# Kernel tuning notes

Measured on AMD Instinct MI355X. Metric: run time of the kernel, lower is better.

Reference implementation:

```python
import jax, jax.numpy as jnp
import numpy as np

# Dimensions (match init_kwargs / input_specs)
N, C_IN, C, H, W = 2, 256, 256, 80, 80
G, KS = 16, 3                 # groups, kernel_size
K = KS * KS                   # sampling points per group
CG = C // G                   # channels per group
PAD, STRIDE, DIL = 1, 1, 1
OFFSET_SCALE = 1.0
EPS = 1e-5                    # BatchNorm2d eps (eval mode)


def setup_inputs() -> dict:
    key = jax.random.key(0)
    ks = jax.random.split(key, 12)
    rn = lambda k, shape, s=0.02: jax.random.normal(k, shape, dtype=jnp.float32) * s
    return {
        "x": jax.random.normal(ks[0], (N, C_IN, H, W), dtype=jnp.float32),
        # Conv(inc, ouc, k=1): 1x1 conv (bias=False) + BN + SiLU
        "w1": rn(ks[1], (C_IN, C)),
        "bn1_g": jnp.ones((C,), jnp.float32), "bn1_b": jnp.zeros((C,), jnp.float32),
        "bn1_m": rn(ks[2], (C,), 0.1),
        "bn1_v": jax.random.uniform(ks[3], (C,), minval=0.5, maxval=1.5, dtype=jnp.float32),
        # DCNv4: value_proj, fused offset_mask, output_proj
        "wv": rn(ks[4], (C, C)), "bv": jnp.zeros((C,), jnp.float32),
        "wom": rn(ks[5], (C, G * K * 3)), "bom": rn(ks[6], (G * K * 3,), 0.1),
        "wo": rn(ks[7], (C, C)), "bo": jnp.zeros((C,), jnp.float32),
        # trailing BatchNorm2d + SiLU
        "bn2_g": jnp.ones((C,), jnp.float32), "bn2_b": jnp.zeros((C,), jnp.float32),
        "bn2_m": rn(ks[8], (C,), 0.1),
        "bn2_v": jax.random.uniform(ks[9], (C,), minval=0.5, maxval=1.5, dtype=jnp.float32),
    }


def _bn(x, g, b, m, v):
    # eval-mode BatchNorm over last (channel) axis
    return (x - m) * jax.lax.rsqrt(v + EPS) * g + b


def _forward(x, w1, bn1_g, bn1_b, bn1_m, bn1_v, wv, bv, wom, bom, wo, bo,
             bn2_g, bn2_b, bn2_m, bn2_v):
    # --- Conv 1x1 + BN + SiLU (channels-last) ---
    h = jnp.einsum('nchw,cd->nhwd', x, w1)                 # (N,H,W,C)
    h = jax.nn.silu(_bn(h, bn1_g, bn1_b, bn1_m, bn1_v))

    # --- DCNv4 ---
    xf = h.reshape(N, H * W, C)
    value = (xf @ wv + bv).reshape(N, H, W, G, CG)         # value projection
    om = (xf @ wom + bom).reshape(N, H, W, G, 3 * K)       # fused offset+mask
    offset = om[..., :2 * K].reshape(N, H, W, G, K, 2) * OFFSET_SCALE  # (x,y) pairs
    mask = om[..., 2 * K:]                                 # (N,H,W,G,K); v4: no softmax

    # sampling pixel coords: p = out_pos*stride - pad + kernel_offset*dil + learned offset
    ky, kx = jnp.meshgrid(jnp.arange(KS), jnp.arange(KS), indexing='ij')
    ky = (ky.reshape(-1) * DIL).astype(jnp.float32)        # (K,)
    kx = (kx.reshape(-1) * DIL).astype(jnp.float32)
    base_y = (jnp.arange(H) * STRIDE - PAD).astype(jnp.float32)
    base_x = (jnp.arange(W) * STRIDE - PAD).astype(jnp.float32)
    py = base_y[None, :, None, None, None] + ky[None, None, None, None, :] + offset[..., 1]
    px = base_x[None, None, :, None, None] + kx[None, None, None, None, :] + offset[..., 0]

    y0 = jnp.floor(py); x0 = jnp.floor(px)
    wy = py - y0;       wx = px - x0
    y0i = y0.astype(jnp.int32); x0i = x0.astype(jnp.int32)
    y1i = y0i + 1;             x1i = x0i + 1

    ni = jnp.arange(N)[:, None, None, None, None]
    gi = jnp.arange(G)[None, None, None, :, None]

    def gather(yi, xi):
        valid = ((yi >= 0) & (yi < H) & (xi >= 0) & (xi < W)).astype(value.dtype)
        v = value[ni, jnp.clip(yi, 0, H - 1), jnp.clip(xi, 0, W - 1), gi]  # (N,H,W,G,K,CG)
        return v, valid

    acc = jnp.zeros((N, H, W, G, CG), dtype=value.dtype)
    for yi, xi, wgt in ((y0i, x0i, (1 - wy) * (1 - wx)),
                        (y0i, x1i, (1 - wy) * wx),
                        (y1i, x0i, wy * (1 - wx)),
                        (y1i, x1i, wy * wx)):
        v, valid = gather(yi, xi)
        acc = acc + jnp.einsum('nhwgk,nhwgkc->nhwgc', mask * wgt * valid, v)

    out = acc.reshape(N, H * W, C) @ wo + bo               # output projection
    out = out.reshape(N, H, W, C)

    # --- BN + SiLU (wrapper tail) ---
    out = jax.nn.silu(_bn(out, bn2_g, bn2_b, bn2_m, bn2_v))
    return jnp.transpose(out, (0, 3, 1, 2))                # (N,C,H,W)


def reference(x, w1, bn1_g, bn1_b, bn1_m, bn1_v, wv, bv, wom, bom, wo, bo,
              bn2_g, bn2_b, bn2_m, bn2_v):
    return _forward(x, w1, bn1_g, bn1_b, bn1_m, bn1_v, wv, bv, wom, bom,
                    wo, bo, bn2_g, bn2_b, bn2_m, bn2_v)
```

## Files before the change

### kernel.cpp

```cpp
#include <hip/hip_runtime.h>
#include <hip/hip_bf16.h>
#include <math.h>

typedef __attribute__((ext_vector_type(8))) short bf16x8;
typedef __attribute__((ext_vector_type(4))) float f32x4;

#define NB   2
#define CC   256
#define HH   80
#define WW   80
#define HWSZ 6400
#define MM   (NB * HWSZ)
#define NCAT 768
#define EPSB 1e-5f

__global__ __launch_bounds__(256) void transpose_x_k(
    const float* __restrict__ in, __hip_bfloat16* __restrict__ outp)
{
    __shared__ float tile[32][33];
    const float* inz = in + (size_t)256 * HWSZ * blockIdx.z;
    __hip_bfloat16* outz = outp + (size_t)HWSZ * 256 * blockIdx.z;
    int bc = blockIdx.x * 32, br = blockIdx.y * 32;
    int tx = threadIdx.x & 31, ty = threadIdx.x >> 5;
#pragma unroll
    for (int i = 0; i < 32; i += 8)
        tile[ty + i][tx] = inz[(size_t)(br + ty + i) * HWSZ + bc + tx];
    __syncthreads();
#pragma unroll
    for (int i = 0; i < 32; i += 8)
        outz[(size_t)(bc + ty + i) * 256 + br + tx] =
            __float2bfloat16(tile[tx][ty + i]);
}

__device__ inline void t32g(const float* __restrict__ in, int inld, int scol0,
                            int ncols, __hip_bfloat16* __restrict__ out,
                            int orow0, int r0, int tid)
{
    __shared__ float tile[32][33];
    int tx = tid & 31, ty = tid >> 5;
#pragma unroll
    for (int i = 0; i < 32; i += 8)
        tile[ty + i][tx] = (tx < ncols)
            ? in[(size_t)(r0 + ty + i) * inld + scol0 + tx] : 0.f;
    __syncthreads();
#pragma unroll
    for (int i = 0; i < 32; i += 8)
        out[(size_t)(orow0 + ty + i) * 256 + r0 + tx] =
            __float2bfloat16(tile[tx][ty + i]);
}

__global__ __launch_bounds__(256) void prep_weights_k(
    const float* __restrict__ w1, const float* __restrict__ wv,
    const float* __restrict__ wom, const float* __restrict__ wo,
    const float* __restrict__ bv, const float* __restrict__ bom,
    __hip_bfloat16* __restrict__ w1T, __hip_bfloat16* __restrict__ BcatT,
    __hip_bfloat16* __restrict__ woT, float* __restrict__ bcat)
{
    int b = blockIdx.x, t = threadIdx.x;
    if (b < 64) {
        t32g(w1, 256, (b >> 3) * 32, 32, w1T, (b >> 3) * 32, (b & 7) * 32, t);
    } else if (b < 128) {
        int b2 = b - 64;
        t32g(wv, 256, (b2 >> 3) * 32, 32, BcatT, (b2 >> 3) * 32, (b2 & 7) * 32, t);
    } else if (b < 192) {
        int b2 = b - 128;
        t32g(wo, 256, (b2 >> 3) * 32, 32, woT, (b2 >> 3) * 32, (b2 & 7) * 32, t);
    } else if (b < 320) {
        int b2 = b - 192;
        int g = b2 >> 3, ct = b2 & 7;
        t32g(wom, 432, g * 27, 27, BcatT + 256 * 256, g * 32, ct * 32, t);
    } else {
        bcat[t] = bv[t];
#pragma unroll
        for (int j = 0; j < 2; ++j) {
            int r = j * 256 + t;
            int g = r >> 5, jj = r & 31;
            bcat[256 + r] = (jj < 27) ? bom[g * 27 + jj] : 0.f;
        }
    }
}

template <int EPI>
__global__ __launch_bounds__(256) void gemm_mfma(
    const short* __restrict__ A, const short* __restrict__ Bt,
    const float* __restrict__ bias,
    const float* __restrict__ bng, const float* __restrict__ bnb,
    const float* __restrict__ bnm, const float* __restrict__ bnv,
    void* __restrict__ Cout, int ldC)
{
    __shared__ __align__(16) char smem[34048];
    short* As = (short*)smem;
    short* Bs = (short*)(smem + 16384);

    const int t = threadIdx.x;
    const int w = t >> 6, l = t & 63;
    const int wr = w >> 1, wc = w & 1;
    const int m0 = blockIdx.x * 128, n0 = blockIdx.y * 128;

    f32x4 acc[4][4] = {};

    for (int k0 = 0; k0 < 256; k0 += 64) {
#pragma unroll
        for (int i = 0; i < 4; ++i) {
            int s = (w << 2) + i;
            int idx = (s << 6) + l;
            int row = idx >> 3, ch = idx & 7;
            const short* ga = A + (size_t)(m0 + row) * 256 + k0 + (ch << 3);
            __builtin_amdgcn_global_load_lds(
                (const __attribute__((address_space(1))) void*)ga,
                (__attribute__((address_space(3))) void*)(As + (s << 9)), 16, 0, 0);
            const short* gb = Bt + (size_t)(n0 + row) * 256 + k0 + (ch << 3);
            __builtin_amdgcn_global_load_lds(
                (const __attribute__((address_space(1))) void*)gb,
                (__attribute__((address_space(3))) void*)(Bs + (s << 9)), 16, 0, 0);
        }
        __syncthreads();
#pragma unroll
        for (int kk = 0; kk < 2; ++kk) {
            bf16x8 af[4], bfr[4];
#pragma unroll
            for (int mi = 0; mi < 4; ++mi)
                af[mi] = *(const bf16x8*)(As + (wr * 64 + mi * 16 + (l & 15)) * 64 +
                                          kk * 32 + ((l >> 4) << 3));
#pragma unroll
            for (int ni = 0; ni < 4; ++ni)
                bfr[ni] = *(const bf16x8*)(Bs + (wc * 64 + ni * 16 + (l & 15)) * 64 +
                                           kk * 32 + ((l >> 4) << 3));
#pragma unroll
            for (int mi = 0; mi < 4; ++mi)
#pragma unroll
                for (int ni = 0; ni < 4; ++ni)
                    acc[mi][ni] = __builtin_amdgcn_mfma_f32_16x16x32_bf16(
                        af[mi], bfr[ni], acc[mi][ni], 0, 0, 0);
        }
        __syncthreads();
    }

    if (EPI == 0) {
#pragma unroll
        for (int ni = 0; ni < 4; ++ni) {
            int chn = n0 + wc * 64 + ni * 16 + (l & 15);
            float bb = bias[chn];
#pragma unroll
            for (int mi = 0; mi < 4; ++mi) {
                int mbase = m0 + wr * 64 + mi * 16 + ((l >> 4) << 2);
#pragma unroll
                for (int j = 0; j < 4; ++j) {
                    float v = acc[mi][ni][j] + bb;
                    ((__hip_bfloat16*)Cout)[(size_t)(mbase + j) * ldC + chn] =
                        __float2bfloat16(v);
                }
            }
        }
    } else if (EPI == 1) {
#pragma unroll
        for (int ni = 0; ni < 4; ++ni) {
            int chn = n0 + wc * 64 + ni * 16 + (l & 15);
            float mu = bnm[chn], iv = rsqrtf(bnv[chn] + EPSB);
            float gm = bng[chn], bt = bnb[chn];
#pragma unroll
            for (int mi = 0; mi < 4; ++mi) {
                int mbase = m0 + wr * 64 + mi * 16 + ((l >> 4) << 2);
#pragma unroll
                for (int j = 0; j < 4; ++j) {
                    float v = acc[mi][ni][j];
                    v = (v - mu) * iv * gm + bt;
                    v = v / (1.f + __expf(-v));
                    ((__hip_bfloat16*)Cout)[(size_t)(mbase + j) * ldC + chn] =
                        __float2bfloat16(v);
                }
            }
        }
    } else {
        float(*CtT)[132] = (float(*)[132])smem;
        const int nimg = m0 / HWSZ;
        const int p0 = m0 % HWSZ;
#pragma unroll
        for (int h2 = 0; h2 < 2; ++h2) {
            if (wc == h2) {
#pragma unroll
                for (int ni = 0; ni < 4; ++ni)
#pragma unroll
                    for (int mi = 0; mi < 4; ++mi)
#pragma unroll
                        for (int j = 0; j < 4; ++j)
                            CtT[ni * 16 + (l & 15)]
                               [wr * 64 + mi * 16 + ((l >> 4) << 2) + j] =
                                   acc[mi][ni][j];
            }
            __syncthreads();
#pragma unroll
            for (int it = 0; it < 8; ++it) {
                int e4 = it * 256 + t;
                int row = e4 >> 5;
                int c4 = e4 & 31;
                int chn = n0 + h2 * 64 + row;
                float bb = bias[chn];
                float mu = bnm[chn], iv = rsqrtf(bnv[chn] + EPSB);
                float gm = bng[chn], bt = bnb[chn];
                f32x4 v = *(f32x4*)&CtT[row][c4 * 4];
#pragma unroll
                for (int j = 0; j < 4; ++j) {
                    float u = v[j] + bb;
                    u = (u - mu) * iv * gm + bt;
                    u = u / (1.f + __expf(-u));
                    v[j] = u;
                }
                *(f32x4*)&((float*)Cout)[(size_t)(nimg * CC + chn) * HWSZ + p0 + c4 * 4] = v;
            }
            __syncthreads();
        }
    }
}

__device__ inline void fma8(float* acc, const __hip_bfloat16* ptr, float wgt)
{
    bf16x8 v = *(const bf16x8*)ptr;
#pragma unroll
    for (int j = 0; j < 8; ++j) {
        union { unsigned u; float f; } cv;
        cv.u = ((unsigned)(unsigned short)v[j]) << 16;
        acc[j] = fmaf(wgt, cv.f, acc[j]);
    }
}

__global__ __launch_bounds__(256) void dcn_sample_k(
    const __hip_bfloat16* __restrict__ C2, __hip_bfloat16* __restrict__ accb)
{
    const int idx = blockIdx.x * 256 + threadIdx.x;
    const int half = idx & 1;
    const int g = (idx >> 1) & 15;
    const int mp = idx >> 5;
    const int p = mp % HWSZ;
    const int n = mp / HWSZ;
    const int y = p / WW, x = p % WW;

    const unsigned* omw =
        (const unsigned*)(C2 + (size_t)mp * NCAT + 256 + g * 32);
    const __hip_bfloat16* vb =
        C2 + (size_t)n * HWSZ * NCAT + g * 16 + half * 8;

    float mk[9];
    {
        unsigned mw[5];
#pragma unroll
        for (int i = 0; i < 5; ++i) mw[i] = omw[9 + i];
#pragma unroll
        for (int i = 0; i < 9; ++i) {
            unsigned w16 = (i & 1) ? (mw[i >> 1] >> 16) : (mw[i >> 1] & 0xffffu);
            union { unsigned u; float f; } cv; cv.u = w16 << 16;
            mk[i] = cv.f;
        }
    }

    float acc[8] = {};
#pragma unroll
    for (int k = 0; k < 9; ++k) {
        unsigned ow = omw[k];
        union { unsigned u; float f; } cx, cy;
        cx.u = (ow & 0xffffu) << 16;
        cy.u = ow & 0xffff0000u;
        float px = (float)(x - 1 + (k % 3)) + cx.f;
        float py = (float)(y - 1 + (k / 3)) + cy.f;
        float fx = floorf(px), fy = floorf(py);
        float wx = px - fx, wy = py - fy;
        int x0 = (int)fx, y0 = (int)fy;
        int x1 = x0 + 1, y1 = y0 + 1;
        float ax0 = ((unsigned)x0 < (unsigned)WW) ? (1.f - wx) : 0.f;
        float ax1 = ((unsigned)x1 < (unsigned)WW) ? wx : 0.f;
        float ay0 = ((unsigned)y0 < (unsigned)HH) ? mk[k] * (1.f - wy) : 0.f;
        float ay1 = ((unsigned)y1 < (unsigned)HH) ? mk[k] * wy : 0.f;
        int xc0 = min(max(x0, 0), WW - 1);
        int xc1 = min(max(x1, 0), WW - 1);
        int yc0 = min(max(y0, 0), HH - 1);
        int yc1 = min(max(y1, 0), HH - 1);
        const __hip_bfloat16* r0 = vb + (size_t)(yc0 * WW) * NCAT;
        const __hip_bfloat16* r1 = vb + (size_t)(yc1 * WW) * NCAT;
        fma8(acc, r0 + (size_t)xc0 * NCAT, ay0 * ax0);
        fma8(acc, r0 + (size_t)xc1 * NCAT, ay0 * ax1);
        fma8(acc, r1 + (size_t)xc0 * NCAT, ay1 * ax0);
        fma8(acc, r1 + (size_t)xc1 * NCAT, ay1 * ax1);
    }

    __hip_bfloat16* op = accb + (size_t)mp * CC + g * 16 + half * 8;
    bf16x8 ov;
#pragma unroll
    for (int j = 0; j < 8; ++j) {
        __hip_bfloat16 b = __float2bfloat16(acc[j]);
        ov[j] = *reinterpret_cast<short*>(&b);
    }
    *(bf16x8*)op = ov;
}

extern "C" void kernel_launch(void* const* d_in, const int* in_sizes, int n_in,
                              void* d_out, int out_size, void* d_ws, size_t ws_size,
                              hipStream_t stream)
{
    const float* x    = (const float*)d_in[0];
    const float* w1   = (const float*)d_in[1];
    const float* bn1g = (const float*)d_in[2];
    const float* bn1b = (const float*)d_in[3];
    const float* bn1m = (const float*)d_in[4];
    const float* bn1v = (const float*)d_in[5];
    const float* wv   = (const float*)d_in[6];
    const float* bv   = (const float*)d_in[7];
    const float* wom  = (const float*)d_in[8];
    const float* bom  = (const float*)d_in[9];
    const float* wo   = (const float*)d_in[10];
    const float* bo   = (const float*)d_in[11];
    const float* bn2g = (const float*)d_in[12];
    const float* bn2b = (const float*)d_in[13];
    const float* bn2m = (const float*)d_in[14];
    const float* bn2v = (const float*)d_in[15];
    float* out = (float*)d_out;

    char* w = (char*)d_ws;
    __hip_bfloat16* xT    = (__hip_bfloat16*)(w);
    __hip_bfloat16* hbuf  = (__hip_bfloat16*)(w + 6553600);
    __hip_bfloat16* C2    = (__hip_bfloat16*)(w + 13107200);
    __hip_bfloat16* accb  = (__hip_bfloat16*)(w + 32768000);
    __hip_bfloat16* w1T   = (__hip_bfloat16*)(w + 39321600);
    __hip_bfloat16* woT   = (__hip_bfloat16*)(w + 39452672);
    __hip_bfloat16* BcatT = (__hip_bfloat16*)(w + 39583744);
    float*          bcat  = (float*)(w + 39976960);

    dim3 blk(256);

    prep_weights_k<<<dim3(321), blk, 0, stream>>>(
        w1, wv, wom, wo, bv, bom, w1T, BcatT, woT, bcat);
    transpose_x_k<<<dim3(200, 8, 2), blk, 0, stream>>>(x, xT);

    gemm_mfma<1><<<dim3(100, 2), blk, 0, stream>>>(
        (const short*)xT, (const short*)w1T, nullptr,
        bn1g, bn1b, bn1m, bn1v, hbuf, CC);
    gemm_mfma<0><<<dim3(100, 6), blk, 0, stream>>>(
        (const short*)hbuf, (const short*)BcatT, bcat,
        nullptr, nullptr, nullptr, nullptr, C2, NCAT);
    dcn_sample_k<<<dim3(MM * 32 / 256), blk, 0, stream>>>(C2, accb);
    gemm_mfma<2><<<dim3(100, 2), blk, 0, stream>>>(
        (const short*)accb, (const short*)woT, bo,
        bn2g, bn2b, bn2m, bn2v, out, 0);
}
```

Before: 151.4 us.

## Double-buffer GEMM K-loop, halve M tile, and give each DCN thread a full group

The MFMA GEMM now uses a 64x128 tile with double-buffered LDS staging, issuing the next K-slice's async global-to-LDS loads before computing the current one, and it launches twice as many blocks. This aims to hide load latency and raise occupancy on a GPU with many compute units, at the cost of more LDS per block and lower per-block reuse. The deformable sampling kernel now has one thread handle all 16 channels of a group instead of two threads handling 8 each. This halves the redundant offset and mask decoding and bilinear index math, but leaves fewer threads in flight.

Result: no change. 150.6 us (-0.5%).

```diff
diff --git a/kernel.cpp b/kernel.cpp
--- a/kernel.cpp
+++ b/kernel.cpp
@@ -88,51 +88,71 @@
     const float* __restrict__ bnm, const float* __restrict__ bnv,
     void* __restrict__ Cout, int ldC)
 {
-    __shared__ __align__(16) char smem[34048];
+    __shared__ __align__(16) char smem[49152];
     short* As = (short*)smem;
     short* Bs = (short*)(smem + 16384);
 
     const int t = threadIdx.x;
     const int w = t >> 6, l = t & 63;
     const int wr = w >> 1, wc = w & 1;
-    const int m0 = blockIdx.x * 128, n0 = blockIdx.y * 128;
-
-    f32x4 acc[4][4] = {};
-
-    for (int k0 = 0; k0 < 256; k0 += 64) {
-#pragma unroll
-        for (int i = 0; i < 4; ++i) {
-            int s = (w << 2) + i;
-            int idx = (s << 6) + l;
-            int row = idx >> 3, ch = idx & 7;
+    const int m0 = blockIdx.x * 64, n0 = blockIdx.y * 128;
+
+    f32x4 acc[2][4] = {};
+
+    auto STAGE = [&](int b, int k0) {
+        short* AsB = As + b * 4096;
+        short* BsB = Bs + b * 8192;
+#pragma unroll
+        for (int i = 0; i < 2; ++i) {
+            int s = (w << 1) + i;
+            int c = (s << 6) + l;
+            int row = c >> 3, ch = c & 7;
             const short* ga = A + (size_t)(m0 + row) * 256 + k0 + (ch << 3);
             __builtin_amdgcn_global_load_lds(
                 (const __attribute__((address_space(1))) void*)ga,
-                (__attribute__((address_space(3))) void*)(As + (s << 9)), 16, 0, 0);
+                (__attribute__((address_space(3))) void*)(AsB + (s << 9)), 16, 0, 0);
+        }
+#pragma unroll
+        for (int i = 0; i < 4; ++i) {
+            int s = (w << 2) + i;
+            int c = (s << 6) + l;
+            int row = c >> 3, ch = c & 7;
             const short* gb = Bt + (size_t)(n0 + row) * 256 + k0 + (ch << 3);
             __builtin_amdgcn_global_load_lds(
                 (const __attribute__((address_space(1))) void*)gb,
-                (__attribute__((address_space(3))) void*)(Bs + (s << 9)), 16, 0, 0);
-        }
-        __syncthreads();
+                (__attribute__((address_space(3))) void*)(BsB + (s << 9)), 16, 0, 0);
+        }
+    };
+
+    auto COMPUTE = [&](int b) {
+        const short* AsB = As + b * 4096;
+        const short* BsB = Bs + b * 8192;
 #pragma unroll
         for (int kk = 0; kk < 2; ++kk) {
-            bf16x8 af[4], bfr[4];
-#pragma unroll
-            for (int mi = 0; mi < 4; ++mi)
-                af[mi] = *(const bf16x8*)(As + (wr * 64 + mi * 16 + (l & 15)) * 64 +
+            bf16x8 af[2], bfr[4];
+#pragma unroll
+            for (int mi = 0; mi < 2; ++mi)
+                af[mi] = *(const bf16x8*)(AsB + (wr * 32 + mi * 16 + (l & 15)) * 64 +
                                           kk * 32 + ((l >> 4) << 3));
 #pragma unroll
             for (int ni = 0; ni < 4; ++ni)
-                bfr[ni] = *(const bf16x8*)(Bs + (wc * 64 + ni * 16 + (l & 15)) * 64 +
+                bfr[ni] = *(const bf16x8*)(BsB + (wc * 64 + ni * 16 + (l & 15)) * 64 +
                                            kk * 32 + ((l >> 4) << 3));
 #pragma unroll
-            for (int mi = 0; mi < 4; ++mi)
+            for (int mi = 0; mi < 2; ++mi)
 #pragma unroll
                 for (int ni = 0; ni < 4; ++ni)
                     acc[mi][ni] = __builtin_amdgcn_mfma_f32_16x16x32_bf16(
                         af[mi], bfr[ni], acc[mi][ni], 0, 0, 0);
         }
+    };
+
+    STAGE(0, 0);
+    __syncthreads();
+#pragma unroll
+    for (int tt = 0; tt < 4; ++tt) {
+        if (tt < 3) STAGE((tt + 1) & 1, (tt + 1) * 64);
+        COMPUTE(tt & 1);
         __syncthreads();
     }
 
@@ -142,8 +162,8 @@
             int chn = n0 + wc * 64 + ni * 16 + (l & 15);
             float bb = bias[chn];
 #pragma unroll
-            for (int mi = 0; mi < 4; ++mi) {
-                int mbase = m0 + wr * 64 + mi * 16 + ((l >> 4) << 2);
+            for (int mi = 0; mi < 2; ++mi) {
+                int mbase = m0 + wr * 32 + mi * 16 + ((l >> 4) << 2);
 #pragma unroll
                 for (int j = 0; j < 4; ++j) {
                     float v = acc[mi][ni][j] + bb;
@@ -159,8 +179,8 @@
             float mu = bnm[chn], iv = rsqrtf(bnv[chn] + EPSB);
             float gm = bng[chn], bt = bnb[chn];
 #pragma unroll
-            for (int mi = 0; mi < 4; ++mi) {
-                int mbase = m0 + wr * 64 + mi * 16 + ((l >> 4) << 2);
+            for (int mi = 0; mi < 2; ++mi) {
+                int mbase = m0 + wr * 32 + mi * 16 + ((l >> 4) << 2);
 #pragma unroll
                 for (int j = 0; j < 4; ++j) {
                     float v = acc[mi][ni][j];
@@ -172,7 +192,7 @@
             }
         }
     } else {
-        float(*CtT)[132] = (float(*)[132])smem;
+        float(*CtT)[68] = (float(*)[68])smem;
         const int nimg = m0 / HWSZ;
         const int p0 = m0 % HWSZ;
 #pragma unroll
@@ -181,19 +201,19 @@
 #pragma unroll
                 for (int ni = 0; ni < 4; ++ni)
 #pragma unroll
-                    for (int mi = 0; mi < 4; ++mi)
+                    for (int mi = 0; mi < 2; ++mi)
 #pragma unroll
                         for (int j = 0; j < 4; ++j)
                             CtT[ni * 16 + (l & 15)]
-                               [wr * 64 + mi * 16 + ((l >> 4) << 2) + j] =
+                               [wr * 32 + mi * 16 + ((l >> 4) << 2) + j] =
                                    acc[mi][ni][j];
             }
             __syncthreads();
 #pragma unroll
-            for (int it = 0; it < 8; ++it) {
+            for (int it = 0; it < 4; ++it) {
                 int e4 = it * 256 + t;
-                int row = e4 >> 5;
-                int c4 = e4 & 31;
+                int row = e4 >> 4;
+                int c4 = e4 & 15;
                 int chn = n0 + h2 * 64 + row;
                 float bb = bias[chn];
                 float mu = bnm[chn], iv = rsqrtf(bnv[chn] + EPSB);
@@ -213,14 +233,21 @@
     }
 }
 
-__device__ inline void fma8(float* acc, const __hip_bfloat16* ptr, float wgt)
-{
-    bf16x8 v = *(const bf16x8*)ptr;
+__device__ inline void fma16(float* acc, const __hip_bfloat16* ptr, float wgt)
+{
+    bf16x8 v0 = *(const bf16x8*)ptr;
+    bf16x8 v1 = *(const bf16x8*)(ptr + 8);
 #pragma unroll
     for (int j = 0; j < 8; ++j) {
         union { unsigned u; float f; } cv;
-        cv.u = ((unsigned)(unsigned short)v[j]) << 16;
+        cv.u = ((unsigned)(unsigned short)v0[j]) << 16;
         acc[j] = fmaf(wgt, cv.f, acc[j]);
+    }
+#pragma unroll
+    for (int j = 0; j < 8; ++j) {
+        union { unsigned u; float f; } cv;
+        cv.u = ((unsigned)(unsigned short)v1[j]) << 16;
+        acc[8 + j] = fmaf(wgt, cv.f, acc[8 + j]);
     }
 }
 
@@ -228,9 +255,8 @@
     const __hip_bfloat16* __restrict__ C2, __hip_bfloat16* __restrict__ accb)
 {
     const int idx = blockIdx.x * 256 + threadIdx.x;
-    const int half = idx & 1;
-    const int g = (idx >> 1) & 15;
-    const int mp = idx >> 5;
+    const int g = idx & 15;
+    const int mp = idx >> 4;
     const int p = mp % HWSZ;
     const int n = mp / HWSZ;
     const int y = p / WW, x = p % WW;
@@ -238,7 +264,7 @@
     const unsigned* omw =
         (const unsigned*)(C2 + (size_t)mp * NCAT + 256 + g * 32);
     const __hip_bfloat16* vb =
-        C2 + (size_t)n * HWSZ * NCAT + g * 16 + half * 8;
+        C2 + (size_t)n * HWSZ * NCAT + g * 16;
 
     float mk[9];
     {
@@ -253,7 +279,7 @@
         }
     }
 
-    float acc[8] = {};
+    float acc[16] = {};
 #pragma unroll
     for (int k = 0; k < 9; ++k) {
         unsigned ow = omw[k];
@@ -276,20 +302,23 @@
         int yc1 = min(max(y1, 0), HH - 1);
         const __hip_bfloat16* r0 = vb + (size_t)(yc0 * WW) * NCAT;
         const __hip_bfloat16* r1 = vb + (size_t)(yc1 * WW) * NCAT;
-        fma8(acc, r0 + (size_t)xc0 * NCAT, ay0 * ax0);
-        fma8(acc, r0 + (size_t)xc1 * NCAT, ay0 * ax1);
-        fma8(acc, r1 + (size_t)xc0 * NCAT, ay1 * ax0);
-        fma8(acc, r1 + (size_t)xc1 * NCAT, ay1 * ax1);
-    }
-
-    __hip_bfloat16* op = accb + (size_t)mp * CC + g * 16 + half * 8;
-    bf16x8 ov;
+        fma16(acc, r0 + (size_t)xc0 * NCAT, ay0 * ax0);
+        fma16(acc, r0 + (size_t)xc1 * NCAT, ay0 * ax1);
+        fma16(acc, r1 + (size_t)xc0 * NCAT, ay1 * ax0);
+        fma16(acc, r1 + (size_t)xc1 * NCAT, ay1 * ax1);
+    }
+
+    __hip_bfloat16* op = accb + (size_t)mp * CC + g * 16;
+    bf16x8 ov0, ov1;
 #pragma unroll
     for (int j = 0; j < 8; ++j) {
-        __hip_bfloat16 b = __float2bfloat16(acc[j]);
-        ov[j] = *reinterpret_cast<short*>(&b);
-    }
-    *(bf16x8*)op = ov;
+        __hip_bfloat16 b0 = __float2bfloat16(acc[j]);
+        __hip_bfloat16 b1 = __float2bfloat16(acc[8 + j]);
+        ov0[j] = *reinterpret_cast<short*>(&b0);
+        ov1[j] = *reinterpret_cast<short*>(&b1);
+    }
+    *(bf16x8*)op = ov0;
+    *(bf16x8*)(op + 8) = ov1;
 }
 
 extern "C" void kernel_launch(void* const* d_in, const int* in_sizes, int n_in,
@@ -330,14 +359,14 @@
         w1, wv, wom, wo, bv, bom, w1T, BcatT, woT, bcat);
     transpose_x_k<<<dim3(200, 8, 2), blk, 0, stream>>>(x, xT);
 
-    gemm_mfma<1><<<dim3(100, 2), blk, 0, stream>>>(
+    gemm_mfma<1><<<dim3(200, 2), blk, 0, stream>>>(
         (const short*)xT, (const short*)w1T, nullptr,
         bn1g, bn1b, bn1m, bn1v, hbuf, CC);
-    gemm_mfma<0><<<dim3(100, 6), blk, 0, stream>>>(
+    gemm_mfma<0><<<dim3(200, 6), blk, 0, stream>>>(
         (const short*)hbuf, (const short*)BcatT, bcat,
         nullptr, nullptr, nullptr, nullptr, C2, NCAT);
-    dcn_sample_k<<<dim3(MM * 32 / 256), blk, 0, stream>>>(C2, accb);
-    gemm_mfma<2><<<dim3(100, 2), blk, 0, stream>>>(
+    dcn_sample_k<<<dim3(MM * 16 / 256), blk, 0, stream>>>(C2, accb);
+    gemm_mfma<2><<<dim3(200, 2), blk, 0, stream>>>(
         (const short*)accb, (const short*)woT, bo,
         bn2g, bn2b, bn2m, bn2v, out, 0);
 }
```
